# Kernel optimization log

Measured on AMD Instinct MI355X. Metric: run time of the kernel, lower is better.

## Reference

```python
import jax, jax.numpy as jnp
import numpy as np

N = 50000   # nodes
E = 800000  # edges (avg out-degree 16)
F = 64      # node features
HID = 128   # hidden size


def _seg(vals, idx, n):
    return jax.ops.segment_sum(vals, idx, num_segments=n)


def dconv(x, src, dst, nw_out, nw_in, W, b, n):
    # Diffusion convolution, K=2. W: (2, K, C, HID); directions: out-walk / in-walk.
    # k=0 term is the identity hop for both directions.
    h = x @ (W[0, 0] + W[1, 0])
    fwd = _seg(nw_out[:, None] * x[src], dst, n)  # (D_out^-1 A) x
    bwd = _seg(nw_in[:, None] * x[dst], src, n)   # (D_in^-1 A^T) x
    return h + fwd @ W[0, 1] + bwd @ W[1, 1] + b


def dcrnn_cell(x, src, dst, nw_out, nw_in, Wz, bz, Wr, br, Wh, bh, n, hid):
    # Single recurrent step with H initialized to zeros (as in the model's single-call use).
    h0 = jnp.zeros((x.shape[0], hid), x.dtype)
    xh = jnp.concatenate([x, h0], axis=-1)
    z = jax.nn.sigmoid(dconv(xh, src, dst, nw_out, nw_in, Wz, bz, n))
    r = jax.nn.sigmoid(dconv(xh, src, dst, nw_out, nw_in, Wr, br, n))
    xrh = jnp.concatenate([x, r * h0], axis=-1)
    h_tilde = jnp.tanh(dconv(xrh, src, dst, nw_out, nw_in, Wh, bh, n))
    return z * h0 + (1.0 - z) * h_tilde


def setup_inputs() -> dict:
    key = jax.random.key(0)
    ks = jax.random.split(key, 20)
    x = jax.random.normal(ks[0], (N, F), jnp.float32)
    edge_index = jax.random.randint(ks[1], (2, E), 0, N, jnp.int32)
    edge_weight = jax.random.uniform(ks[2], (E,), jnp.float32)

    c1 = F + HID
    c2 = HID + HID

    def mkW(k, c):
        return jax.random.normal(k, (2, 2, c, HID), jnp.float32) / np.float32(np.sqrt(c))

    inp = {
        "x": x,
        "edge_index": edge_index,
        "edge_weight": edge_weight,
        "W1_z": mkW(ks[3], c1), "b1_z": jnp.zeros((HID,), jnp.float32),
        "W1_r": mkW(ks[4], c1), "b1_r": jnp.zeros((HID,), jnp.float32),
        "W1_h": mkW(ks[5], c1), "b1_h": jnp.zeros((HID,), jnp.float32),
        "W2_z": mkW(ks[6], c2), "b2_z": jnp.zeros((HID,), jnp.float32),
        "W2_r": mkW(ks[7], c2), "b2_r": jnp.zeros((HID,), jnp.float32),
        "W2_h": mkW(ks[8], c2), "b2_h": jnp.zeros((HID,), jnp.float32),
        "Wlin": jax.random.normal(ks[9], (HID, 1), jnp.float32) / np.float32(np.sqrt(HID)),
        "blin": jnp.zeros((1,), jnp.float32),
    }
    return inp


def reference(x, edge_index, edge_weight,
              W1_z, b1_z, W1_r, b1_r, W1_h, b1_h,
              W2_z, b2_z, W2_r, b2_r, W2_h, b2_h,
              Wlin, blin):
    src, dst = edge_index[0], edge_index[1]
    n = x.shape[0]
    # Random-walk normalization of edge weights (out- and in-degree), safe reciprocal.
    deg_out = _seg(edge_weight, src, n)
    deg_in = _seg(edge_weight, dst, n)
    nw_out = edge_weight * jnp.where(deg_out[src] > 0, 1.0 / deg_out[src], 0.0)
    nw_in = edge_weight * jnp.where(deg_in[dst] > 0, 1.0 / deg_in[dst], 0.0)

    h = dcrnn_cell(x, src, dst, nw_out, nw_in, W1_z, b1_z, W1_r, b1_r, W1_h, b1_h, n, HID)
    h = dcrnn_cell(h, src, dst, nw_out, nw_in, W2_z, b2_z, W2_r, b2_r, W2_h, b2_h, n, HID)
    # dropout=0.0 -> identity; final linear head -> (N, 1)
    return h @ Wlin + blin
```

## Files before the change

### kernel.cpp

```cpp
#include <hip/hip_runtime.h>
#include <hip/hip_fp16.h>
#include <cstdint>
#include <type_traits>

#define NN 50000
#define NE 800000
#define CAP 48
#define NPART 391
#define BINCAP 2560
#define CHUNK 4096

typedef unsigned short u16;
typedef unsigned int u32;
typedef unsigned long long u64;
typedef u16 u16x8 __attribute__((ext_vector_type(8)));
typedef __bf16 bf16x8 __attribute__((ext_vector_type(8)));
typedef float f32x4 __attribute__((ext_vector_type(4)));

__device__ __forceinline__ u16 f2bf(float f) {
  u32 u = __float_as_uint(f);
  u = (u + 0x7fff + ((u >> 16) & 1)) >> 16;
  return (u16)u;
}
__device__ __forceinline__ float bf2f(u32 b) { return __uint_as_float(b << 16); }

__launch_bounds__(512)
__global__ void k_bin(const int* __restrict__ src, const int* __restrict__ dst,
                      const float* __restrict__ ew, int2* __restrict__ bins,
                      u32* __restrict__ binCnt) {
  const int dir = blockIdx.y;
  const int e0 = blockIdx.x * CHUNK;
  const int n = min(CHUNK, NE - e0);
  const int* key = dir ? src : dst;
  const int* oth = dir ? dst : src;
  __shared__ u32 cnt[512];
  __shared__ u32 scan[512];
  __shared__ u32 gbase[512];
  __shared__ int2 ent[CHUNK];
  __shared__ u32 dsts[CHUNK];
  const int t = threadIdx.x;
  cnt[t] = 0;
  __syncthreads();

  int pj[8], mj[8], wj[8];
  u32 oj[8];
#pragma unroll
  for (int j = 0; j < 8; ++j) {
    const int i = j * 512 + t;
    pj[j] = -1;
    if (i < n) {
      const int e = e0 + i;
      const int k = key[e];
      pj[j] = k >> 7;
      mj[j] = ((k & 127) << 16) | oth[e];
      wj[j] = __float_as_int(ew[e]);
      oj[j] = atomicAdd(&cnt[pj[j]], 1u);
    }
  }
  __syncthreads();
  scan[t] = cnt[t];
  __syncthreads();
  for (int s = 1; s < 512; s <<= 1) {
    u32 v = (t >= s) ? scan[t - s] : 0;
    __syncthreads();
    scan[t] += v;
    __syncthreads();
  }
  if (t < NPART) gbase[t] = cnt[t] ? atomicAdd(&binCnt[dir * NPART + t], cnt[t]) : 0;
  __syncthreads();
#pragma unroll
  for (int j = 0; j < 8; ++j) {
    if (pj[j] >= 0) {
      const int p = pj[j];
      const u32 slot = scan[p] - cnt[p] + oj[j];
      ent[slot] = make_int2(mj[j], wj[j]);
      const u32 go = gbase[p] + oj[j];
      dsts[slot] = (go < BINCAP) ? (u32)p * BINCAP + go : 0xFFFFFFFFu;
    }
  }
  __syncthreads();
  int2* bdir = bins + (size_t)dir * NPART * BINCAP;
  for (int i = t; i < n; i += 512) {
    const u32 d = dsts[i];
    if (d != 0xFFFFFFFFu) bdir[d] = ent[i];
  }
}

__launch_bounds__(512)
__global__ void k_scatter2(const int2* __restrict__ bins, const u32* __restrict__ binCnt,
                           u32* __restrict__ bucketF, u32* __restrict__ bucketB,
                           u32* __restrict__ cntNF, u32* __restrict__ cntNB,
                           float* __restrict__ invF, float* __restrict__ invB) {
  const int p = blockIdx.x, dir = blockIdx.y;
  __shared__ u64 cd[128];
  __shared__ u32 stage[128 * CAP];
  const int t = threadIdx.x;
  if (t < 128) cd[t] = 0;
  __syncthreads();
  const int2* bin = bins + ((size_t)dir * NPART + p) * BINCAP;
  int bn = binCnt[dir * NPART + p];
  if (bn > BINCAP) bn = BINCAP;
  for (int i = t; i < bn; i += 512) {
    const int2 e = bin[i];
    const int ln = e.x >> 16;
    const float w = __int_as_float(e.y);
    const u64 inc = (1ULL << 32) | (u64)__float2uint_rn(w * 16777216.0f);
    const u32 slot = (u32)(atomicAdd(&cd[ln], inc) >> 32);
    const __half hw = __float2half_rn(w);
    if (slot < CAP)
      stage[ln * CAP + slot] = ((u32)(e.x & 0xffff) << 16) | (u32)__half_as_ushort(hw);
  }
  __syncthreads();
  u32* bucket = dir ? bucketB : bucketF;
  for (int i = t; i < 128 * CAP; i += 512) {
    const int ln = i / CAP, s = i % CAP;
    const int g = p * 128 + ln;
    u32 c = (u32)(cd[ln] >> 32);
    if (c > CAP) c = CAP;
    if (g < NN && s < (int)c) bucket[(size_t)g * CAP + s] = stage[i];
  }
  if (t < 128) {
    const int g = p * 128 + t;
    if (g < NN) {
      u32 c = (u32)(cd[t] >> 32);
      const u32 dfix = (u32)cd[t];
      if (c > CAP) c = CAP;
      (dir ? cntNB : cntNF)[g] = c;
      (dir ? invB : invF)[g] = dfix ? 16777216.f / (float)dfix : 0.f;
    }
  }
}

__global__ void k_cast(const float* __restrict__ x, u16* __restrict__ xb) {
  int i = (blockIdx.x * 256 + threadIdx.x) * 8;
  if (i >= NN * 64) return;
  float4 v0 = *(const float4*)&x[i];
  float4 v1 = *(const float4*)&x[i + 4];
  u16x8 o;
  o[0] = f2bf(v0.x); o[1] = f2bf(v0.y); o[2] = f2bf(v0.z); o[3] = f2bf(v0.w);
  o[4] = f2bf(v1.x); o[5] = f2bf(v1.y); o[6] = f2bf(v1.z); o[7] = f2bf(v1.w);
  *(u16x8*)&xb[i] = o;
}

template <int C>
__global__ void k_pack(const float* __restrict__ Wz, const float* __restrict__ Wh,
                       u16* __restrict__ WpT) {
  constexpr int K = 3 * C;
  constexpr int CIN = (C == 64) ? 192 : 256;
  int col = blockIdx.x;
  int k = threadIdx.x;
  int part = k / C, c = k % C, o = col & 127;
  const float* W = (col < 128) ? Wz : Wh;
  float v;
  if (part == 0)      v = W[(0 * CIN + c) * 128 + o] + W[(2 * CIN + c) * 128 + o];
  else if (part == 1) v = W[(1 * CIN + c) * 128 + o];
  else                v = W[(3 * CIN + c) * 128 + o];
  WpT[col * K + k] = f2bf(v);
}

template <int C>
__launch_bounds__(256)
__global__ void k_gather(const u16* __restrict__ x, const u32* __restrict__ cntNF,
                         const u32* __restrict__ bucketF, const u32* __restrict__ cntNB,
                         const u32* __restrict__ bucketB, const float* __restrict__ invF,
                         const float* __restrict__ invB, u16* __restrict__ fwd,
                         u16* __restrict__ bwd) {
  constexpr int G = C / 8;
  constexpr int NG = 64 / G;
  const int node = blockIdx.x * 4 + (threadIdx.x >> 6);
  if (node >= NN) return;
  const int lane = threadIdx.x & 63;
  const int g = lane / G;
  const int p = lane % G;
  const uint4* xa = (const uint4*)x;

  const int nF = cntNF[node];
  const int nB = cntNB[node];

  u32 eF = 0, eB = 0;
  if (lane < nF) eF = __builtin_nontemporal_load(&bucketF[(size_t)node * CAP + lane]);
  if (lane < nB) eB = __builtin_nontemporal_load(&bucketB[(size_t)node * CAP + lane]);
  const int idxF = eF >> 16;
  const int idxB = eB >> 16;
  const float wFl =
      __half2float(__ushort_as_half((u16)(eF & 0xffff))) * invB[idxF];
  const float wBl =
      __half2float(__ushort_as_half((u16)(eB & 0xffff))) * invF[idxB];

  float accF[8], accB[8];
#pragma unroll
  for (int j = 0; j < 8; ++j) { accF[j] = 0.f; accB[j] = 0.f; }

  const int mm = nF > nB ? nF : nB;
#pragma unroll 2
  for (int i = 0; i < mm; i += NG) {
    const int ii = i + g;
    const int mF = __shfl(idxF, ii);
    const float wF = __shfl(wFl, ii);
    const int mB = __shfl(idxB, ii);
    const float wB = __shfl(wBl, ii);
    uint4 vF = {0, 0, 0, 0}, vB = {0, 0, 0, 0};
    if (ii < nF) vF = xa[(u32)mF * G + p];
    if (ii < nB) vB = xa[(u32)mB * G + p];
    accF[0] += wF * bf2f(vF.x & 0xffff); accF[1] += wF * bf2f(vF.x >> 16);
    accF[2] += wF * bf2f(vF.y & 0xffff); accF[3] += wF * bf2f(vF.y >> 16);
    accF[4] += wF * bf2f(vF.z & 0xffff); accF[5] += wF * bf2f(vF.z >> 16);
    accF[6] += wF * bf2f(vF.w & 0xffff); accF[7] += wF * bf2f(vF.w >> 16);
    accB[0] += wB * bf2f(vB.x & 0xffff); accB[1] += wB * bf2f(vB.x >> 16);
    accB[2] += wB * bf2f(vB.y & 0xffff); accB[3] += wB * bf2f(vB.y >> 16);
    accB[4] += wB * bf2f(vB.z & 0xffff); accB[5] += wB * bf2f(vB.z >> 16);
    accB[6] += wB * bf2f(vB.w & 0xffff); accB[7] += wB * bf2f(vB.w >> 16);
  }

#pragma unroll
  for (int s = 32; s >= G; s >>= 1) {
#pragma unroll
    for (int j = 0; j < 8; ++j) {
      accF[j] += __shfl_xor(accF[j], s);
      accB[j] += __shfl_xor(accB[j], s);
    }
  }

  if (g < 2) {
    const float* a = g ? accB : accF;
    u16* o = g ? bwd : fwd;
    u16x8 pv;
#pragma unroll
    for (int j = 0; j < 8; ++j) pv[j] = f2bf(a[j]);
    *(u16x8*)&o[(size_t)node * C + p * 8] = pv;
  }
}

template <int C, bool HEAD>
__launch_bounds__(256)
__global__ void k_gemm(const u16* __restrict__ P0, const u16* __restrict__ P1,
                       const u16* __restrict__ P2, const u16* __restrict__ WpT,
                       const float* __restrict__ bz, const float* __restrict__ bh,
                       void* __restrict__ outv, const float* __restrict__ wlin,
                       const float* __restrict__ blin) {
  constexpr int K = 3 * C;
  __shared__ char smem[40960];
  u16* As = (u16*)smem;
  u16* Bs = (u16*)(smem + 8192);
  const int t = threadIdx.x;
  const int w = t >> 6;
  const int l = t & 63;
  const int lc = l & 15, lq = l >> 4;
  const int bm = blockIdx.x * 64;

  f32x4 acc[4][4];
#pragma unroll
  for (int mi = 0; mi < 4; ++mi)
#pragma unroll
    for (int ni = 0; ni < 4; ++ni) acc[mi][ni] = (f32x4){0.f, 0.f, 0.f, 0.f};

  for (int kt = 0; kt < K / 64; ++kt) {
    const int k0 = kt * 64;
    const u16* P;
    int lc0;
    if (C == 64) { P = (kt == 0) ? P0 : (kt == 1 ? P1 : P2); lc0 = 0; }
    else         { P = (kt < 2) ? P0 : (kt < 4 ? P1 : P2);   lc0 = (kt & 1) * 64; }
    {
      const int row = t >> 2;
      const int gr = bm + row;
      const int g0 = (t & 3) * 2;
      u16x8 v0 = {0, 0, 0, 0, 0, 0, 0, 0}, v1 = v0;
      if (gr < NN) {
        const u16* s = &P[(size_t)gr * C + lc0 + g0 * 8];
        v0 = *(const u16x8*)s;
        v1 = *(const u16x8*)(s + 8);
      }
      *(u16x8*)&As[row * 64 + ((g0 ^ (row & 7)) * 8)] = v0;
      *(u16x8*)&As[row * 64 + (((g0 + 1) ^ (row & 7)) * 8)] = v1;
    }
    {
      const int col = t;
      const u16* s = &WpT[(size_t)col * K + k0];
#pragma unroll
      for (int g = 0; g < 8; ++g) {
        u16x8 v = *(const u16x8*)(s + g * 8);
        *(u16x8*)&Bs[col * 64 + ((g ^ (col & 7)) * 8)] = v;
      }
    }
    __syncthreads();
#pragma unroll
    for (int kk = 0; kk < 2; ++kk) {
      bf16x8 af[4], bfr[4];
#pragma unroll
      for (int mi = 0; mi < 4; ++mi) {
        const int row = 16 * mi + lc;
        const int g = kk * 4 + lq;
        af[mi] = *(const bf16x8*)&As[row * 64 + ((g ^ (row & 7)) * 8)];
      }
#pragma unroll
      for (int ni = 0; ni < 4; ++ni) {
        const int col = 64 * w + 16 * ni + lc;
        const int g = kk * 4 + lq;
        bfr[ni] = *(const bf16x8*)&Bs[col * 64 + ((g ^ (col & 7)) * 8)];
      }
#pragma unroll
      for (int mi = 0; mi < 4; ++mi)
#pragma unroll
        for (int ni = 0; ni < 4; ++ni)
          acc[mi][ni] = __builtin_amdgcn_mfma_f32_16x16x32_bf16(af[mi], bfr[ni],
                                                                acc[mi][ni], 0, 0, 0);
    }
    __syncthreads();
  }

  float* Hs = (float*)smem;
  if (w >= 2) {
#pragma unroll
    for (int mi = 0; mi < 4; ++mi)
#pragma unroll
      for (int ni = 0; ni < 4; ++ni) {
        const int c2 = 64 * (w - 2) + 16 * ni + lc;
        const float bhv = bh[c2];
#pragma unroll
        for (int r = 0; r < 4; ++r)
          Hs[(16 * mi + 4 * lq + r) * 129 + c2] = tanhf(acc[mi][ni][r] + bhv);
      }
  }
  float* outS = (float*)(smem + 33280);
  if (HEAD && t < 64) outS[t] = 0.f;
  __syncthreads();

  if (w < 2) {
    if constexpr (!HEAD) {
      u16* out = (u16*)outv;
#pragma unroll
      for (int mi = 0; mi < 4; ++mi)
#pragma unroll
        for (int ni = 0; ni < 4; ++ni) {
          const int col = 64 * w + 16 * ni + lc;
          const float bzv = bz[col];
#pragma unroll
          for (int r = 0; r < 4; ++r) {
            const int row = 16 * mi + 4 * lq + r;
            const int gr = bm + row;
            const float z = 1.f / (1.f + __expf(-(acc[mi][ni][r] + bzv)));
            const float hv = (1.f - z) * Hs[row * 129 + col];
            if (gr < NN) out[(size_t)gr * 128 + col] = f2bf(hv);
          }
        }
    } else {
#pragma unroll
      for (int mi = 0; mi < 4; ++mi)
#pragma unroll
        for (int r = 0; r < 4; ++r) {
          const int row = 16 * mi + 4 * lq + r;
          float part = 0.f;
#pragma unroll
          for (int ni = 0; ni < 4; ++ni) {
            const int col = 64 * w + 16 * ni + lc;
            const float z = 1.f / (1.f + __expf(-(acc[mi][ni][r] + bz[col])));
            part += (1.f - z) * Hs[row * 129 + col] * wlin[col];
          }
          part += __shfl_xor(part, 1);
          part += __shfl_xor(part, 2);
          part += __shfl_xor(part, 4);
          part += __shfl_xor(part, 8);
          if (lc == 0) atomicAdd(&outS[row], part);
        }
    }
  }
  if constexpr (HEAD) {
    __syncthreads();
    if (t < 64) {
      const int gr = bm + t;
      if (gr < NN) ((float*)outv)[gr] = outS[t] + blin[0];
    }
  }
}

extern "C" void kernel_launch(void* const* d_in, const int* in_sizes, int n_in,
                              void* d_out, int out_size, void* d_ws, size_t ws_size,
                              hipStream_t stream) {
  const float* x    = (const float*)d_in[0];
  const int*   ei   = (const int*)d_in[1];
  const float* ew   = (const float*)d_in[2];
  const float* W1z  = (const float*)d_in[3];
  const float* b1z  = (const float*)d_in[4];
  const float* W1h  = (const float*)d_in[7];
  const float* b1h  = (const float*)d_in[8];
  const float* W2z  = (const float*)d_in[9];
  const float* b2z  = (const float*)d_in[10];
  const float* W2h  = (const float*)d_in[13];
  const float* b2h  = (const float*)d_in[14];
  const float* Wlin = (const float*)d_in[15];
  const float* blin = (const float*)d_in[16];
  const int* src = ei;
  const int* dst = ei + NE;

  char* p8 = (char*)d_ws;
  auto alloc = [&](size_t bytes) { char* r = p8; p8 += (bytes + 15) & ~15ull; return r; };
  u32*   binCnt  = (u32*)alloc(2 * NPART * 4);
  int2*  bins    = (int2*)alloc((size_t)2 * NPART * BINCAP * 8);
  u32*   bucketF = (u32*)alloc((size_t)NN * CAP * 4);
  u32*   bucketB = (u32*)alloc((size_t)NN * CAP * 4);
  u32*   cntNF   = (u32*)alloc(NN * 4);
  u32*   cntNB   = (u32*)alloc(NN * 4);
  float* invF    = (float*)alloc(NN * 4);
  float* invB    = (float*)alloc(NN * 4);
  u16*   WpT1 = (u16*)alloc(256 * 192 * 2);
  u16*   WpT2 = (u16*)alloc(256 * 384 * 2);
  u16*   xb   = (u16*)alloc((size_t)NN * 64 * 2);
  u16*   h1   = (u16*)alloc((size_t)NN * 128 * 2);
  u16*   fwd1 = (u16*)alloc((size_t)NN * 64 * 2);
  u16*   bwd1 = (u16*)alloc((size_t)NN * 64 * 2);
  u16*   bwd2 = (u16*)alloc((size_t)NN * 128 * 2);
  u16*   fwd2 = fwd1;

  hipMemsetAsync(binCnt, 0, 2 * NPART * 4, stream);

  const dim3 binGrid((NE + CHUNK - 1) / CHUNK, 2);
  k_bin<<<binGrid, 512, 0, stream>>>(src, dst, ew, bins, binCnt);
  k_scatter2<<<dim3(NPART, 2), 512, 0, stream>>>(bins, binCnt, bucketF, bucketB,
                                                 cntNF, cntNB, invF, invB);
  k_pack<64><<<256, 192, 0, stream>>>(W1z, W1h, WpT1);
  k_pack<128><<<256, 384, 0, stream>>>(W2z, W2h, WpT2);
  k_cast<<<(NN * 64 / 8 + 255) / 256, 256, 0, stream>>>(x, xb);

  const int nb4 = (NN + 3) / 4;
  const int gblocks = (NN + 63) / 64;

  k_gather<64><<<nb4, 256, 0, stream>>>(xb, cntNF, bucketF, cntNB, bucketB, invF, invB,
                                        fwd1, bwd1);
  k_gemm<64, false><<<gblocks, 256, 0, stream>>>(xb, fwd1, bwd1, WpT1, b1z, b1h, h1,
                                                 nullptr, nullptr);
  k_gather<128><<<nb4, 256, 0, stream>>>(h1, cntNF, bucketF, cntNB, bucketB, invF, invB,
                                         fwd2, bwd2);
  k_gemm<128, true><<<gblocks, 256, 0, stream>>>(h1, fwd2, bwd2, WpT2, b2z, b2h,
                                                 d_out, Wlin, blin);
}
```

Measured before the change: 251.6 us.

## Split layer-1 gather into two source-index phases for cache locality

The bucket build now counts each node's neighbours separately for source indices below and above a split point and lays them out so the low-index neighbours come first. Layer 1's gather then runs as two passes: the first handles only low-index sources and writes fp32 partial sums, and the second handles high-index sources, adds the partials and writes bf16. The goal is to keep each pass's gathered feature working set small enough to stay in cache. The cost is an extra kernel launch, an extra fp32 partial round trip through memory, and a second pass over the edges in the scatter kernel.

Result: slower. 280.4 us (+11.4%).

```diff
diff --git a/kernel.cpp b/kernel.cpp
--- a/kernel.cpp
+++ b/kernel.cpp
@@ -1,7 +1,6 @@
 #include <hip/hip_runtime.h>
 #include <hip/hip_fp16.h>
 #include <cstdint>
-#include <type_traits>
 
 #define NN 50000
 #define NE 800000
@@ -9,6 +8,7 @@
 #define NPART 391
 #define BINCAP 2560
 #define CHUNK 4096
+#define PHSPLIT 25000
 
 typedef unsigned short u16;
 typedef unsigned int u32;
@@ -92,10 +92,11 @@
                            u32* __restrict__ cntNF, u32* __restrict__ cntNB,
                            float* __restrict__ invF, float* __restrict__ invB) {
   const int p = blockIdx.x, dir = blockIdx.y;
-  __shared__ u64 cd[128];
+  __shared__ u32 degfix[128];
+  __shared__ u32 pcnt[128][2];
   __shared__ u32 stage[128 * CAP];
   const int t = threadIdx.x;
-  if (t < 128) cd[t] = 0;
+  if (t < 128) { degfix[t] = 0; pcnt[t][0] = 0; pcnt[t][1] = 0; }
   __syncthreads();
   const int2* bin = bins + ((size_t)dir * NPART + p) * BINCAP;
   int bn = binCnt[dir * NPART + p];
@@ -103,31 +104,45 @@
   for (int i = t; i < bn; i += 512) {
     const int2 e = bin[i];
     const int ln = e.x >> 16;
+    const int idx = e.x & 0xffff;
     const float w = __int_as_float(e.y);
-    const u64 inc = (1ULL << 32) | (u64)__float2uint_rn(w * 16777216.0f);
-    const u32 slot = (u32)(atomicAdd(&cd[ln], inc) >> 32);
-    const __half hw = __float2half_rn(w);
+    atomicAdd(&pcnt[ln][idx >= PHSPLIT], 1u);
+    atomicAdd(&degfix[ln], __float2uint_rn(w * 16777216.0f));
+  }
+  __syncthreads();
+  if (t < 128) {
+    const int g = p * 128 + t;
+    u32 lo = pcnt[t][0], hi = pcnt[t][1];
+    u32 n = lo + hi;
+    u32 nlo = lo < CAP ? lo : CAP;
+    if (n > CAP) n = CAP;
+    if (g < NN) {
+      (dir ? cntNB : cntNF)[g] = (nlo << 8) | n;
+      const u32 dfix = degfix[t];
+      (dir ? invB : invF)[g] = dfix ? 16777216.f / (float)dfix : 0.f;
+    }
+    pcnt[t][0] = 0;
+    pcnt[t][1] = lo;
+  }
+  __syncthreads();
+  for (int i = t; i < bn; i += 512) {
+    const int2 e = bin[i];
+    const int ln = e.x >> 16;
+    const int idx = e.x & 0xffff;
+    const float w = __int_as_float(e.y);
+    const u32 slot = atomicAdd(&pcnt[ln][idx >= PHSPLIT], 1u);
     if (slot < CAP)
-      stage[ln * CAP + slot] = ((u32)(e.x & 0xffff) << 16) | (u32)__half_as_ushort(hw);
+      stage[ln * CAP + slot] =
+          ((u32)idx << 16) | (u32)__half_as_ushort(__float2half_rn(w));
   }
   __syncthreads();
   u32* bucket = dir ? bucketB : bucketF;
   for (int i = t; i < 128 * CAP; i += 512) {
     const int ln = i / CAP, s = i % CAP;
     const int g = p * 128 + ln;
-    u32 c = (u32)(cd[ln] >> 32);
+    u32 c = pcnt[ln][1];
     if (c > CAP) c = CAP;
     if (g < NN && s < (int)c) bucket[(size_t)g * CAP + s] = stage[i];
-  }
-  if (t < 128) {
-    const int g = p * 128 + t;
-    if (g < NN) {
-      u32 c = (u32)(cd[t] >> 32);
-      const u32 dfix = (u32)cd[t];
-      if (c > CAP) c = CAP;
-      (dir ? cntNB : cntNF)[g] = c;
-      (dir ? invB : invF)[g] = dfix ? 16777216.f / (float)dfix : 0.f;
-    }
   }
 }
 
@@ -158,15 +173,15 @@
   WpT[col * K + k] = f2bf(v);
 }
 
-template <int C>
+template <int PHASE>
 __launch_bounds__(256)
-__global__ void k_gather(const u16* __restrict__ x, const u32* __restrict__ cntNF,
-                         const u32* __restrict__ bucketF, const u32* __restrict__ cntNB,
-                         const u32* __restrict__ bucketB, const float* __restrict__ invF,
-                         const float* __restrict__ invB, u16* __restrict__ fwd,
-                         u16* __restrict__ bwd) {
-  constexpr int G = C / 8;
-  constexpr int NG = 64 / G;
+__global__ void k_gather64p(const u16* __restrict__ x, const u32* __restrict__ cntNF,
+                            const u32* __restrict__ bucketF, const u32* __restrict__ cntNB,
+                            const u32* __restrict__ bucketB, const float* __restrict__ invF,
+                            const float* __restrict__ invB, float* __restrict__ fwdf,
+                            float* __restrict__ bwdf, u16* __restrict__ fwd,
+                            u16* __restrict__ bwd) {
+  constexpr int G = 8, NG = 8;
   const int node = blockIdx.x * 4 + (threadIdx.x >> 6);
   if (node >= NN) return;
   const int lane = threadIdx.x & 63;
@@ -174,18 +189,20 @@
   const int p = lane % G;
   const uint4* xa = (const uint4*)x;
 
-  const int nF = cntNF[node];
-  const int nB = cntNB[node];
-
-  u32 eF = 0, eB = 0;
-  if (lane < nF) eF = __builtin_nontemporal_load(&bucketF[(size_t)node * CAP + lane]);
-  if (lane < nB) eB = __builtin_nontemporal_load(&bucketB[(size_t)node * CAP + lane]);
-  const int idxF = eF >> 16;
-  const int idxB = eB >> 16;
-  const float wFl =
-      __half2float(__ushort_as_half((u16)(eF & 0xffff))) * invB[idxF];
-  const float wBl =
-      __half2float(__ushort_as_half((u16)(eB & 0xffff))) * invF[idxB];
+  const u32 cwF = cntNF[node], cwB = cntNB[node];
+  const int nFa = cwF & 0xff, nLoF = (cwF >> 8) & 0xff;
+  const int nBa = cwB & 0xff, nLoB = (cwB >> 8) & 0xff;
+  const int sF = PHASE ? nLoF : 0, eF = PHASE ? nFa : nLoF;
+  const int sB = PHASE ? nLoB : 0, eB = PHASE ? nBa : nLoB;
+  const int nF = eF - sF, nB = eB - sB;
+
+  u32 eFe = 0, eBe = 0;
+  if (lane < nF) eFe = __builtin_nontemporal_load(&bucketF[(size_t)node * CAP + sF + lane]);
+  if (lane < nB) eBe = __builtin_nontemporal_load(&bucketB[(size_t)node * CAP + sB + lane]);
+  const int idxF = eFe >> 16;
+  const int idxB = eBe >> 16;
+  const float wFl = __half2float(__ushort_as_half((u16)(eFe & 0xffff))) * invB[idxF];
+  const float wBl = __half2float(__ushort_as_half((u16)(eBe & 0xffff))) * invF[idxB];
 
   float accF[8], accB[8];
 #pragma unroll
@@ -222,12 +239,93 @@
   }
 
   if (g < 2) {
+    float a[8];
+#pragma unroll
+    for (int j = 0; j < 8; ++j) a[j] = g ? accB[j] : accF[j];
+    float* of = g ? bwdf : fwdf;
+    if constexpr (PHASE == 0) {
+      *(float4*)&of[(size_t)node * 64 + p * 8] = (float4){a[0], a[1], a[2], a[3]};
+      *(float4*)&of[(size_t)node * 64 + p * 8 + 4] = (float4){a[4], a[5], a[6], a[7]};
+    } else {
+      float4 p0 = *(const float4*)&of[(size_t)node * 64 + p * 8];
+      float4 p1 = *(const float4*)&of[(size_t)node * 64 + p * 8 + 4];
+      a[0] += p0.x; a[1] += p0.y; a[2] += p0.z; a[3] += p0.w;
+      a[4] += p1.x; a[5] += p1.y; a[6] += p1.z; a[7] += p1.w;
+      u16* o = g ? bwd : fwd;
+      u16x8 pv;
+#pragma unroll
+      for (int j = 0; j < 8; ++j) pv[j] = f2bf(a[j]);
+      *(u16x8*)&o[(size_t)node * 64 + p * 8] = pv;
+    }
+  }
+}
+
+__launch_bounds__(256)
+__global__ void k_gather128(const u16* __restrict__ x, const u32* __restrict__ cntNF,
+                            const u32* __restrict__ bucketF, const u32* __restrict__ cntNB,
+                            const u32* __restrict__ bucketB, const float* __restrict__ invF,
+                            const float* __restrict__ invB, u16* __restrict__ fwd,
+                            u16* __restrict__ bwd) {
+  constexpr int G = 16, NG = 4;
+  const int node = blockIdx.x * 4 + (threadIdx.x >> 6);
+  if (node >= NN) return;
+  const int lane = threadIdx.x & 63;
+  const int g = lane / G;
+  const int p = lane % G;
+  const uint4* xa = (const uint4*)x;
+
+  const int nF = cntNF[node] & 0xff;
+  const int nB = cntNB[node] & 0xff;
+
+  u32 eFe = 0, eBe = 0;
+  if (lane < nF) eFe = __builtin_nontemporal_load(&bucketF[(size_t)node * CAP + lane]);
+  if (lane < nB) eBe = __builtin_nontemporal_load(&bucketB[(size_t)node * CAP + lane]);
+  const int idxF = eFe >> 16;
+  const int idxB = eBe >> 16;
+  const float wFl = __half2float(__ushort_as_half((u16)(eFe & 0xffff))) * invB[idxF];
+  const float wBl = __half2float(__ushort_as_half((u16)(eBe & 0xffff))) * invF[idxB];
+
+  float accF[8], accB[8];
+#pragma unroll
+  for (int j = 0; j < 8; ++j) { accF[j] = 0.f; accB[j] = 0.f; }
+
+  const int mm = nF > nB ? nF : nB;
+#pragma unroll 2
+  for (int i = 0; i < mm; i += NG) {
+    const int ii = i + g;
+    const int mF = __shfl(idxF, ii);
+    const float wF = __shfl(wFl, ii);
+    const int mB = __shfl(idxB, ii);
+    const float wB = __shfl(wBl, ii);
+    uint4 vF = {0, 0, 0, 0}, vB = {0, 0, 0, 0};
+    if (ii < nF) vF = xa[(u32)mF * G + p];
+    if (ii < nB) vB = xa[(u32)mB * G + p];
+    accF[0] += wF * bf2f(vF.x & 0xffff); accF[1] += wF * bf2f(vF.x >> 16);
+    accF[2] += wF * bf2f(vF.y & 0xffff); accF[3] += wF * bf2f(vF.y >> 16);
+    accF[4] += wF * bf2f(vF.z & 0xffff); accF[5] += wF * bf2f(vF.z >> 16);
+    accF[6] += wF * bf2f(vF.w & 0xffff); accF[7] += wF * bf2f(vF.w >> 16);
+    accB[0] += wB * bf2f(vB.x & 0xffff); accB[1] += wB * bf2f(vB.x >> 16);
+    accB[2] += wB * bf2f(vB.y & 0xffff); accB[3] += wB * bf2f(vB.y >> 16);
+    accB[4] += wB * bf2f(vB.z & 0xffff); accB[5] += wB * bf2f(vB.z >> 16);
+    accB[6] += wB * bf2f(vB.w & 0xffff); accB[7] += wB * bf2f(vB.w >> 16);
+  }
+
+#pragma unroll
+  for (int s = 32; s >= G; s >>= 1) {
+#pragma unroll
+    for (int j = 0; j < 8; ++j) {
+      accF[j] += __shfl_xor(accF[j], s);
+      accB[j] += __shfl_xor(accB[j], s);
+    }
+  }
+
+  if (g < 2) {
     const float* a = g ? accB : accF;
     u16* o = g ? bwd : fwd;
     u16x8 pv;
 #pragma unroll
     for (int j = 0; j < 8; ++j) pv[j] = f2bf(a[j]);
-    *(u16x8*)&o[(size_t)node * C + p * 8] = pv;
+    *(u16x8*)&o[(size_t)node * 128 + p * 8] = pv;
   }
 }
 
@@ -409,6 +507,8 @@
   u16*   fwd1 = (u16*)alloc((size_t)NN * 64 * 2);
   u16*   bwd1 = (u16*)alloc((size_t)NN * 64 * 2);
   u16*   bwd2 = (u16*)alloc((size_t)NN * 128 * 2);
+  float* fwdf = (float*)alloc((size_t)NN * 64 * 4);
+  float* bwdf = (float*)alloc((size_t)NN * 64 * 4);
   u16*   fwd2 = fwd1;
 
   hipMemsetAsync(binCnt, 0, 2 * NPART * 4, stream);
@@ -424,12 +524,14 @@
   const int nb4 = (NN + 3) / 4;
   const int gblocks = (NN + 63) / 64;
 
-  k_gather<64><<<nb4, 256, 0, stream>>>(xb, cntNF, bucketF, cntNB, bucketB, invF, invB,
-                                        fwd1, bwd1);
+  k_gather64p<0><<<nb4, 256, 0, stream>>>(xb, cntNF, bucketF, cntNB, bucketB, invF, invB,
+                                          fwdf, bwdf, fwd1, bwd1);
+  k_gather64p<1><<<nb4, 256, 0, stream>>>(xb, cntNF, bucketF, cntNB, bucketB, invF, invB,
+                                          fwdf, bwdf, fwd1, bwd1);
   k_gemm<64, false><<<gblocks, 256, 0, stream>>>(xb, fwd1, bwd1, WpT1, b1z, b1h, h1,
                                                  nullptr, nullptr);
-  k_gather<128><<<nb4, 256, 0, stream>>>(h1, cntNF, bucketF, cntNB, bucketB, invF, invB,
-                                         fwd2, bwd2);
+  k_gather128<<<nb4, 256, 0, stream>>>(h1, cntNF, bucketF, cntNB, bucketB, invF, invB,
+                                       fwd2, bwd2);
   k_gemm<128, true><<<gblocks, 256, 0, stream>>>(h1, fwd2, bwd2, WpT2, b2z, b2h,
                                                  d_out, Wlin, blin);
 }
```
